# Optimization experiments

Measured on AMD Instinct MI355X. Metric: run time of the kernel, lower is better.

The kernel has to match this reference:

```python
import jax, jax.numpy as jnp
import numpy as np

ASSIGN_TEMP = 0.1
BATCH_SIZE = 16
NUM_PROTOTYPES = 1024
EMBD_DIM = 512


def setup_inputs() -> dict:
    key = jax.random.key(0)
    k1, k2 = jax.random.split(key)
    feature_maps = jax.random.normal(k1, (BATCH_SIZE, EMBD_DIM, 64, 64), dtype=jnp.float32)
    prototypes = jax.random.normal(k2, (1, NUM_PROTOTYPES, EMBD_DIM), dtype=jnp.float32)
    return {"feature_maps": feature_maps, "prototypes": prototypes}


def reference(feature_maps, prototypes):
    # assign_nearest_clusters
    bs, c, h, w = feature_maps.shape
    K = prototypes.shape[1]
    # [N, c] pixel embeddings (channels-last flatten, as movedim(1,3).reshape)
    x = feature_maps.transpose(0, 2, 3, 1).reshape(-1, c)
    p = prototypes[0]  # [K, c]
    d2 = (jnp.sum(x * x, axis=1, keepdims=True)
          + jnp.sum(p * p, axis=1)[None, :]
          - 2.0 * (x @ p.T))
    dist = jnp.sqrt(jnp.maximum(d2, 0.0))  # [N, K]
    sims = jax.nn.softmax(-dist / ASSIGN_TEMP, axis=1)  # [N, K]
    sims = sims.reshape(bs, h, w, K).transpose(0, 3, 1, 2)  # [bs, K, h, w]
    nearest = jnp.argmax(sims, axis=1)  # [bs, h, w]
    onehot = jax.nn.one_hot(nearest, K, dtype=jnp.int32)  # [bs, h, w, K]
    counts = onehot.sum(axis=(1, 2))  # [bs, K] pixels per prototype
    mask = (counts > 3).sum()
    return sims, mask.astype(jnp.float32) / BATCH_SIZE
```

## Files before the change

kernel.cpp:

```cpp
#include <hip/hip_runtime.h>
#include <hip/hip_bf16.h>
#include <stdint.h>

typedef _Float16 f16x8 __attribute__((ext_vector_type(8)));
typedef _Float16 f16x4 __attribute__((ext_vector_type(4)));
typedef _Float16 f16x2 __attribute__((ext_vector_type(2)));
typedef float    f32x4 __attribute__((ext_vector_type(4)));

#define NPROTO 1024
#define EMB    512
#define NB     16
#define HW     4096
#define NPIX   (NB * HW)
#define INV_TEMP 10.0f

__global__ void prep_protos(const float* __restrict__ proto,
                            _Float16* __restrict__ Ph,
                            float* __restrict__ pnorm) {
    int k = blockIdx.x;
    int t = threadIdx.x;
    const float* src = proto + (size_t)k * EMB + t * 8;
    float4 v0 = ((const float4*)src)[0];
    float4 v1 = ((const float4*)src)[1];
    float sq = v0.x*v0.x + v0.y*v0.y + v0.z*v0.z + v0.w*v0.w
             + v1.x*v1.x + v1.y*v1.y + v1.z*v1.z + v1.w*v1.w;
    f16x8 h;
    h[0] = (_Float16)v0.x; h[1] = (_Float16)v0.y; h[2] = (_Float16)v0.z; h[3] = (_Float16)v0.w;
    h[4] = (_Float16)v1.x; h[5] = (_Float16)v1.y; h[6] = (_Float16)v1.z; h[7] = (_Float16)v1.w;
    *(f16x8*)(Ph + (size_t)k * EMB + t * 8) = h;
#pragma unroll
    for (int m = 1; m < 64; m <<= 1) sq += __shfl_xor(sq, m);
    if (t == 0) pnorm[k] = sq;
}

__global__ void zero_counts(int* __restrict__ counts) {
    int i = blockIdx.x * blockDim.x + threadIdx.x;
    if (i < NB * NPROTO) counts[i] = 0;
}

__global__ __launch_bounds__(1024)
void p0_transpose(const float* __restrict__ fm, _Float16* __restrict__ Xh,
                  float* __restrict__ xn) {
    __shared__ __align__(16) unsigned char tile[128 * 1024];
    __shared__ float xnpart[32 * 128];

    const int t   = threadIdx.x;
    const int b   = blockIdx.x >> 5;
    const int px0 = (blockIdx.x & 31) * 128;

    float sq0 = 0.f, sq1 = 0.f, sq2 = 0.f, sq3 = 0.f;
    const int p4 = t & 31;
#pragma unroll
    for (int j = 0; j < 16; ++j) {
        int f4 = j * 1024 + t;
        int c  = f4 >> 5;
        float4 v = *(const float4*)(fm + ((size_t)b * EMB + c) * HW + px0 + p4 * 4);
        sq0 += v.x * v.x; sq1 += v.y * v.y; sq2 += v.z * v.z; sq3 += v.w * v.w;
#pragma unroll
        for (int i = 0; i < 4; ++i) {
            int p = p4 * 4 + i;
            float val = (i == 0) ? v.x : (i == 1) ? v.y : (i == 2) ? v.z : v.w;
            int slot = (c >> 3) ^ ((p >> 2) & 63);
            *(_Float16*)(tile + p * 1024 + slot * 16 + (c & 7) * 2) = (_Float16)val;
        }
    }
    xnpart[(t >> 5) * 128 + p4 * 4 + 0] = sq0;
    xnpart[(t >> 5) * 128 + p4 * 4 + 1] = sq1;
    xnpart[(t >> 5) * 128 + p4 * 4 + 2] = sq2;
    xnpart[(t >> 5) * 128 + p4 * 4 + 3] = sq3;
    __syncthreads();

    if (t < 128) {
        float s = 0.f;
#pragma unroll
        for (int g = 0; g < 32; ++g) s += xnpart[g * 128 + t];
        xn[b * HW + px0 + t] = s;
    }
    const int wid = t >> 6, lane = t & 63;
#pragma unroll
    for (int rr = 0; rr < 8; ++rr) {
        int p = wid * 8 + rr;
        int phys = lane ^ ((p >> 2) & 63);
        f16x8 v = *(const f16x8*)(tile + p * 1024 + phys * 16);
        *(f16x8*)(Xh + ((size_t)b * HW + px0 + p) * EMB + lane * 8) = v;
    }
}

__global__ __launch_bounds__(512, 4)
void pA_gemm(const _Float16* __restrict__ Xh, const _Float16* __restrict__ Ph,
             const float* __restrict__ pnorm, const float* __restrict__ xn,
             _Float16* __restrict__ e_out, float4* __restrict__ pstat) {
    __shared__ __align__(16) unsigned char smem[74752];
    float* pn = (float*)(smem + 73728);
    float* redmax = (float*)(smem);
    float* redsum = (float*)(smem + 2048);
    float* argv_  = (float*)(smem + 4096);
    int*   argk_  = (int*)(smem + 6144);

    const int t    = threadIdx.x;
    const int lane = t & 63, wid = t >> 6;
    const int kw   = wid >> 1, pw = wid & 1;
    const int lrow = lane >> 4, lcol = lane & 15;

    const int bid   = blockIdx.x;
    const int pt    = bid >> 2, slice = bid & 3;
    const int gpx0  = pt * 128;
    const int k0g   = slice * 256;

    if (t < 256) pn[t] = pnorm[k0g + t];

    f32x4 acc[4][4];
#pragma unroll
    for (int i = 0; i < 4; ++i)
#pragma unroll
        for (int j = 0; j < 4; ++j)
#pragma unroll
            for (int e = 0; e < 4; ++e) acc[i][j][e] = 0.0f;

    auto stage = [&](int buf, int ks) {
        const int c0 = ks * 32;
        unsigned char* base = smem + buf * 24576;
#pragma unroll
        for (int h = 0; h < 2; ++h) {
            int r  = wid * 32 + h * 16 + (lane >> 2);
            int cg = (lane & 3) ^ ((r >> 1) & 3);
            __builtin_amdgcn_global_load_lds(
                (const __attribute__((address_space(1))) void*)(Ph + (size_t)(k0g + r) * EMB + c0 + cg * 8),
                (__attribute__((address_space(3))) void*)(base + wid * 2048 + h * 1024),
                16, 0, 0);
        }
        int px  = wid * 16 + (lane >> 2);
        int cgb = (lane & 3) ^ ((px >> 1) & 3);
        __builtin_amdgcn_global_load_lds(
            (const __attribute__((address_space(1))) void*)(Xh + (size_t)(gpx0 + px) * EMB + c0 + cgb * 8),
            (__attribute__((address_space(3))) void*)(base + 16384 + wid * 1024),
            16, 0, 0);
    };

    stage(0, 0);
    stage(1, 1);
    asm volatile("s_waitcnt vmcnt(3)" ::: "memory");
    __builtin_amdgcn_s_barrier();
    __builtin_amdgcn_sched_barrier(0);

#pragma unroll
    for (int ks = 0; ks < 16; ++ks) {
        const int buf = ks % 3;
        if (ks < 14) stage((ks + 2) % 3, ks + 2);
        const unsigned char* Ab = smem + buf * 24576;
        const unsigned char* Bb = Ab + 16384;

        f16x8 bf[4];
#pragma unroll
        for (int nf = 0; nf < 4; ++nf) {
            int px = pw * 64 + nf * 16 + lcol;
            bf[nf] = *(const f16x8*)(Bb + px * 64 + ((lrow ^ ((px >> 1) & 3)) << 4));
        }
        __builtin_amdgcn_s_setprio(1);
#pragma unroll
        for (int mf = 0; mf < 4; ++mf) {
            int r = kw * 64 + mf * 16 + lcol;
            f16x8 af = *(const f16x8*)(Ab + r * 64 + ((lrow ^ ((r >> 1) & 3)) << 4));
#pragma unroll
            for (int nf = 0; nf < 4; ++nf)
                acc[mf][nf] = __builtin_amdgcn_mfma_f32_16x16x32_f16(af, bf[nf], acc[mf][nf], 0, 0, 0);
        }
        __builtin_amdgcn_s_setprio(0);

        if (ks < 14) {
            asm volatile("s_waitcnt vmcnt(3)" ::: "memory");
        } else if (ks == 14) {
            asm volatile("s_waitcnt vmcnt(0)" ::: "memory");
        }
        if (ks < 15) {
            __builtin_amdgcn_s_barrier();
            __builtin_amdgcn_sched_barrier(0);
        }
    }

    float xnv[4];
#pragma unroll
    for (int nf = 0; nf < 4; ++nf) xnv[nf] = xn[gpx0 + pw * 64 + nf * 16 + lcol];

    float lmax[4] = {-1e30f, -1e30f, -1e30f, -1e30f};
    float lav[4]  = {-1e30f, -1e30f, -1e30f, -1e30f};
    int   lak[4]  = {0, 0, 0, 0};
#pragma unroll
    for (int mf = 0; mf < 4; ++mf)
#pragma unroll
        for (int nf = 0; nf < 4; ++nf)
#pragma unroll
            for (int j = 0; j < 4; ++j) {
                int kl = kw * 64 + mf * 16 + lrow * 4 + j;
                float d2 = xnv[nf] + pn[kl] - 2.0f * acc[mf][nf][j];
                float lg = -INV_TEMP * sqrtf(fmaxf(d2, 0.0f));
                acc[mf][nf][j] = lg;
                if (lg > lav[nf]) { lav[nf] = lg; lak[nf] = kl; }
                lmax[nf] = fmaxf(lmax[nf], lg);
            }
#pragma unroll
    for (int nf = 0; nf < 4; ++nf)
#pragma unroll
        for (int m = 16; m <= 32; m <<= 1) {
            float ov = __shfl_xor(lav[nf], m);
            int   ok = __shfl_xor(lak[nf], m);
            if (ov > lav[nf] || (ov == lav[nf] && ok < lak[nf])) { lav[nf] = ov; lak[nf] = ok; }
            lmax[nf] = fmaxf(lmax[nf], __shfl_xor(lmax[nf], m));
        }

    __syncthreads();
    if (lane < 16)
#pragma unroll
        for (int nf = 0; nf < 4; ++nf) {
            int px = pw * 64 + nf * 16 + lane;
            redmax[kw * 128 + px] = lmax[nf];
            argv_[kw * 128 + px]  = lav[nf];
            argk_[kw * 128 + px]  = lak[nf];
        }
    __syncthreads();

#pragma unroll
    for (int nf = 0; nf < 4; ++nf) {
        int px = pw * 64 + nf * 16 + lcol;
        float m = -1e30f;
#pragma unroll
        for (int w = 0; w < 4; ++w) m = fmaxf(m, redmax[w * 128 + px]);
        float s = 0.0f;
#pragma unroll
        for (int mf = 0; mf < 4; ++mf)
#pragma unroll
            for (int j = 0; j < 4; ++j) {
                float e = __expf(acc[mf][nf][j] - m);
                acc[mf][nf][j] = e;
                s += e;
            }
        s += __shfl_xor(s, 16);
        s += __shfl_xor(s, 32);
        if (lane < 16) redsum[kw * 128 + nf * 16 + pw * 64 + lane] = s;
    }

#pragma unroll
    for (int mf = 0; mf < 4; ++mf)
#pragma unroll
        for (int nf = 0; nf < 4; ++nf) {
            int px = pw * 64 + nf * 16 + lcol;
            int kl = kw * 64 + mf * 16 + lrow * 4;
            f16x4 h;
#pragma unroll
            for (int j = 0; j < 4; ++j) h[j] = (_Float16)acc[mf][nf][j];
            *(f16x4*)(e_out + (size_t)(gpx0 + px) * NPROTO + k0g + kl) = h;
        }
    __syncthreads();

    if (kw == 0 && lane < 16) {
#pragma unroll
        for (int nf = 0; nf < 4; ++nf) {
            int px = pw * 64 + nf * 16 + lane;
            float m = -1e30f, s = 0.0f, av = -1e30f;
            int ak = 0;
#pragma unroll
            for (int w = 0; w < 4; ++w) {
                m = fmaxf(m, redmax[w * 128 + px]);
                s += redsum[w * 128 + px];
                float v = argv_[w * 128 + px];
                int   k = argk_[w * 128 + px];
                if (v > av || (v == av && k < ak)) { av = v; ak = k; }
            }
            float4 st;
            st.x = m; st.y = s; st.z = __int_as_float(k0g + ak); st.w = 0.0f;
            pstat[(size_t)slice * NPIX + gpx0 + px] = st;
        }
    }
}

__global__ void pC_combine(const float4* __restrict__ pstat, float* __restrict__ scale,
                           int* __restrict__ counts) {
    int px = blockIdx.x * 256 + threadIdx.x;
    if (px >= NPIX) return;
    float4 s0 = pstat[px];
    float4 s1 = pstat[NPIX + px];
    float4 s2 = pstat[2 * NPIX + px];
    float4 s3 = pstat[3 * NPIX + px];
    float m = fmaxf(fmaxf(s0.x, s1.x), fmaxf(s2.x, s3.x));
    float e0 = __expf(s0.x - m), e1 = __expf(s1.x - m);
    float e2 = __expf(s2.x - m), e3 = __expf(s3.x - m);
    float S = s0.y * e0 + s1.y * e1 + s2.y * e2 + s3.y * e3;
    float rs = 1.0f / S;
    scale[px * 4 + 0] = e0 * rs;
    scale[px * 4 + 1] = e1 * rs;
    scale[px * 4 + 2] = e2 * rs;
    scale[px * 4 + 3] = e3 * rs;
    float bv = s0.x; int bk = __float_as_int(s0.z);
    if (s1.x > bv) { bv = s1.x; bk = __float_as_int(s1.z); }
    if (s2.x > bv) { bv = s2.x; bk = __float_as_int(s2.z); }
    if (s3.x > bv) { bv = s3.x; bk = __float_as_int(s3.z); }
    int b = px >> 12;
    atomicAdd(&counts[b * NPROTO + bk], 1);
}

__global__ __launch_bounds__(1024)
void pB_emit(const _Float16* __restrict__ e, const float* __restrict__ scale,
             float* __restrict__ out) {
    __shared__ float tile[64 * 261];

    const int t = threadIdx.x;
    const int px0g = blockIdx.x * 256;
    const int b = px0g >> 12, hw0 = px0g & 4095;
    const int lpx = t >> 2, kq = t & 3;
    const int orow = t >> 4, oseg = t & 15;

    for (int kc = 0; kc < 16; ++kc) {
        int slice = kc >> 2;
        float sc = scale[(px0g + lpx) * 4 + slice];
        const _Float16* src = e + (size_t)(px0g + lpx) * NPROTO + kc * 64 + kq * 16;
        f16x8 h0 = *(const f16x8*)(src);
        f16x8 h1 = *(const f16x8*)(src + 8);
        if (kc) __syncthreads();
#pragma unroll
        for (int j = 0; j < 8; ++j) {
            tile[(kq * 16 + j) * 261 + lpx]     = (float)h0[j] * sc;
            tile[(kq * 16 + 8 + j) * 261 + lpx] = (float)h1[j] * sc;
        }
        __syncthreads();
        size_t obase = (size_t)b * NPROTO * HW + (size_t)(kc * 64 + orow) * HW + hw0 + oseg * 16;
#pragma unroll
        for (int i = 0; i < 4; ++i) {
            float4 v;
            v.x = tile[orow * 261 + oseg * 16 + i * 4 + 0];
            v.y = tile[orow * 261 + oseg * 16 + i * 4 + 1];
            v.z = tile[orow * 261 + oseg * 16 + i * 4 + 2];
            v.w = tile[orow * 261 + oseg * 16 + i * 4 + 3];
            *(float4*)(out + obase + i * 4) = v;
        }
    }
}

__global__ void finalize(const int* __restrict__ counts, float* __restrict__ out) {
    int t = threadIdx.x;
    int local = 0;
    for (int i = t; i < NB * NPROTO; i += 256) local += (counts[i] > 3) ? 1 : 0;
#pragma unroll
    for (int m = 1; m < 64; m <<= 1) local += __shfl_xor(local, m);
    __shared__ int wsum[4];
    if ((t & 63) == 0) wsum[t >> 6] = local;
    __syncthreads();
    if (t == 0) out[(size_t)NPIX * NPROTO] = (float)(wsum[0] + wsum[1] + wsum[2] + wsum[3]) / 16.0f;
}

__global__ __launch_bounds__(1024, 1)
void assign_fused(const float* __restrict__ fm, const _Float16* __restrict__ Ph,
                  const float* __restrict__ pnorm, int* __restrict__ counts,
                  float* __restrict__ out) {
    __shared__ __align__(16) unsigned char smem[143360];
    unsigned char* Abuf = smem;
    unsigned char* Bbuf = smem + 131072;
    float* pn           = (float*)(smem + 139264);
    float* redmax = (float*)(smem);
    float* redsum = (float*)(smem + 4096);
    float* argv_  = (float*)(smem + 8192);
    int*   argk_  = (int*)  (smem + 12288);
    float* xnsum  = (float*)(smem + 16384);
    float* xn     = (float*)(smem + 20480);

    const int t    = threadIdx.x;
    const int lane = t & 63, wid = t >> 6;
    const int lrow = lane >> 4, lcol = lane & 15;
    const int n0  = blockIdx.x * 64;
    const int b   = n0 >> 12;
    const int hw0 = n0 & 4095;

    pn[t] = pnorm[t];
    f32x4 acc[4][4];
#pragma unroll
    for (int i = 0; i < 4; ++i)
#pragma unroll
        for (int j = 0; j < 4; ++j)
#pragma unroll
            for (int e = 0; e < 4; ++e) acc[i][j][e] = 0.0f;

    const int bpx = t & 63;
    const int bc  = (t >> 6) << 1;
    const float* fmB = fm + (size_t)b * EMB * HW + hw0 + bpx;
    float sq = 0.0f;
    float bv0, bv1;

    auto stageA = [&](int cur, int ks) {
        const int c0 = ks * 32;
#pragma unroll
        for (int p = 0; p < 4; ++p) {
            int k  = p * 256 + wid * 16 + (lane >> 2);
            int cg = (lane & 3) ^ (k & 3);
            __builtin_amdgcn_global_load_lds(
                (const __attribute__((address_space(1))) void*)(Ph + (size_t)k * EMB + c0 + cg * 8),
                (__attribute__((address_space(3))) void*)(Abuf + cur * 65536 + p * 16384 + wid * 1024),
                16, 0, 0);
        }
    };
    auto loadB = [&](int ks) {
        const float* p0 = fmB + (size_t)(ks * 32 + bc) * HW;
        bv0 = p0[0]; bv1 = p0[HW];
    };
    auto writeB = [&](int cur) {
        sq += bv0 * bv0 + bv1 * bv1;
        f16x2 h; h[0] = (_Float16)bv0; h[1] = (_Float16)bv1;
        int slot = (bc >> 3) ^ (bpx & 3);
        *(f16x2*)(Bbuf + cur * 4096 + bpx * 64 + (slot << 4) + (bc & 7) * 2) = h;
    };

    stageA(0, 0); loadB(0); writeB(0);
    __syncthreads();
    int cur = 0;
    for (int ks = 0; ks < 16; ++ks) {
        if (ks < 15) { stageA(cur ^ 1, ks + 1); loadB(ks + 1); }
        f16x8 bf[4];
#pragma unroll
        for (int nf = 0; nf < 4; ++nf) {
            int px = nf * 16 + lcol;
            bf[nf] = *(const f16x8*)(Bbuf + cur * 4096 + px * 64 + ((lrow ^ (px & 3)) << 4));
        }
#pragma unroll
        for (int mf = 0; mf < 4; ++mf) {
            int r = wid * 64 + mf * 16 + lcol;
            f16x8 af = *(const f16x8*)(Abuf + cur * 65536 + r * 64 + ((lrow ^ (r & 3)) << 4));
#pragma unroll
            for (int nf = 0; nf < 4; ++nf)
                acc[mf][nf] = __builtin_amdgcn_mfma_f32_16x16x32_f16(af, bf[nf], acc[mf][nf], 0, 0, 0);
        }
        if (ks < 15) writeB(cur ^ 1);
        __syncthreads();
        cur ^= 1;
    }

    xnsum[(t >> 6) * 64 + bpx] = sq;
    __syncthreads();
    if (t < 64) {
        float s = 0.0f;
#pragma unroll
        for (int g = 0; g < 16; ++g) s += xnsum[g * 64 + t];
        xn[t] = s;
    }
    __syncthreads();

    float xnv[4];
#pragma unroll
    for (int nf = 0; nf < 4; ++nf) xnv[nf] = xn[nf * 16 + lcol];
    float lmax[4] = {-1e30f, -1e30f, -1e30f, -1e30f};
    float lav[4]  = {-1e30f, -1e30f, -1e30f, -1e30f};
    int   lak[4]  = {0, 0, 0, 0};
#pragma unroll
    for (int mf = 0; mf < 4; ++mf)
#pragma unroll
        for (int nf = 0; nf < 4; ++nf)
#pragma unroll
            for (int j = 0; j < 4; ++j) {
                int kidx = wid * 64 + mf * 16 + lrow * 4 + j;
                float d2 = xnv[nf] + pn[kidx] - 2.0f * acc[mf][nf][j];
                float lg = -INV_TEMP * sqrtf(fmaxf(d2, 0.0f));
                acc[mf][nf][j] = lg;
                if (lg > lav[nf]) { lav[nf] = lg; lak[nf] = kidx; }
                lmax[nf] = fmaxf(lmax[nf], lg);
            }
#pragma unroll
    for (int nf = 0; nf < 4; ++nf)
#pragma unroll
        for (int m = 16; m <= 32; m <<= 1) {
            float ov = __shfl_xor(lav[nf], m);
            int   ok = __shfl_xor(lak[nf], m);
            if (ov > lav[nf] || (ov == lav[nf] && ok < lak[nf])) { lav[nf] = ov; lak[nf] = ok; }
            lmax[nf] = fmaxf(lmax[nf], __shfl_xor(lmax[nf], m));
        }
    if (lane < 16)
#pragma unroll
        for (int nf = 0; nf < 4; ++nf) {
            int idx = wid * 64 + nf * 16 + lane;
            redmax[idx] = lmax[nf]; argv_[idx] = lav[nf]; argk_[idx] = lak[nf];
        }
    __syncthreads();

#pragma unroll
    for (int nf = 0; nf < 4; ++nf) {
        int px = nf * 16 + lcol;
        float gm = -1e30f, gav = -1e30f;
        int gak = 0;
#pragma unroll
        for (int w = 0; w < 16; ++w) {
            gm = fmaxf(gm, redmax[w * 64 + px]);
            float av = argv_[w * 64 + px];
            int   ak = argk_[w * 64 + px];
            if (av > gav || (av == gav && ak < gak)) { gav = av; gak = ak; }
        }
        if (wid == 0 && lane < 16) atomicAdd(&counts[b * NPROTO + gak], 1);
        float s = 0.0f;
#pragma unroll
        for (int mf = 0; mf < 4; ++mf)
#pragma unroll
            for (int j = 0; j < 4; ++j) {
                float e = __expf(acc[mf][nf][j] - gm);
                acc[mf][nf][j] = e;
                s += e;
            }
        s += __shfl_xor(s, 16);
        s += __shfl_xor(s, 32);
        if (lane < 16) redsum[wid * 64 + nf * 16 + lane] = s;
    }
    __syncthreads();

    const size_t obase = (size_t)b * NPROTO * HW + hw0;
#pragma unroll
    for (int nf = 0; nf < 4; ++nf) {
        int px = nf * 16 + lcol;
        float s = 0.0f;
#pragma unroll
        for (int w = 0; w < 16; ++w) s += redsum[w * 64 + px];
        float inv = 1.0f / s;
#pragma unroll
        for (int mf = 0; mf < 4; ++mf)
#pragma unroll
            for (int j = 0; j < 4; ++j) {
                int kidx = wid * 64 + mf * 16 + lrow * 4 + j;
                out[obase + (size_t)kidx * HW + px] = acc[mf][nf][j] * inv;
            }
    }
}

extern "C" void kernel_launch(void* const* d_in, const int* in_sizes, int n_in,
                              void* d_out, int out_size, void* d_ws, size_t ws_size,
                              hipStream_t stream) {
    const float* fm    = (const float*)d_in[0];
    const float* proto = (const float*)d_in[1];
    float* out = (float*)d_out;

    char* ws = (char*)d_ws;
    const size_t E_OFF  = 0;
    const size_t XH_OFF = 134217728;
    const size_t PS_OFF = XH_OFF + 67108864;
    const size_t SC_OFF = PS_OFF + 4194304;
    const size_t XN_OFF = SC_OFF + 1048576;
    const size_t PH_OFF = XN_OFF + 262144;
    const size_t PN_OFF = PH_OFF + 1048576;
    const size_t CT_OFF = PN_OFF + 4096;
    const size_t NEED   = CT_OFF + 65536;

    if (ws_size >= NEED) {
        _Float16* e     = (_Float16*)(ws + E_OFF);
        _Float16* Xh    = (_Float16*)(ws + XH_OFF);
        float4*   pstat = (float4*)(ws + PS_OFF);
        float*    scale = (float*)(ws + SC_OFF);
        float*    xn    = (float*)(ws + XN_OFF);
        _Float16* Ph    = (_Float16*)(ws + PH_OFF);
        float*    pnorm = (float*)(ws + PN_OFF);
        int*      counts= (int*)(ws + CT_OFF);

        prep_protos<<<NPROTO, 64, 0, stream>>>(proto, Ph, pnorm);
        zero_counts<<<(NB * NPROTO + 255) / 256, 256, 0, stream>>>(counts);
        p0_transpose<<<NB * 32, 1024, 0, stream>>>(fm, Xh, xn);
        pA_gemm<<<(NPIX / 128) * 4, 512, 0, stream>>>(Xh, Ph, pnorm, xn, e, pstat);
        pC_combine<<<NPIX / 256, 256, 0, stream>>>(pstat, scale, counts);
        pB_emit<<<NPIX / 256, 1024, 0, stream>>>(e, scale, out);
        finalize<<<1, 256, 0, stream>>>(counts, out);
    } else {
        _Float16* Ph    = (_Float16*)ws;
        float*    pnorm = (float*)(ws + (size_t)NPROTO * EMB * 2);
        int*      counts= (int*)(ws + (size_t)NPROTO * EMB * 2 + 4096);
        prep_protos<<<NPROTO, 64, 0, stream>>>(proto, Ph, pnorm);
        zero_counts<<<(NB * NPROTO + 255) / 256, 256, 0, stream>>>(counts);
        assign_fused<<<NPIX / 64, 1024, 0, stream>>>(fm, Ph, pnorm, counts, out);
        finalize<<<1, 256, 0, stream>>>(counts, out);
    }
}
```

Baseline: 329.2 us.

## Enlarge GEMM tile to 256x256 with 64-wide K steps and phased staging

Reworks the distance GEMM to compute a 256-pixel by 256-prototype tile per 512-thread block, with a 64-element K step, double-buffered LDS and XOR swizzling. Each K step is split into four phases that interleave global-to-LDS staging of the next tile with MFMA work on the current one. The intent is more operand reuse per LDS load and fewer blocks and barriers. The softmax max is now taken from the argmax value rather than a separate max reduction, and the square root uses an inline v_sqrt. In exchange the block needs about 129 KB of LDS and twice the accumulator registers, which limits occupancy to two blocks.

```diff
diff --git a/kernel.cpp b/kernel.cpp
--- a/kernel.cpp
+++ b/kernel.cpp
@@ -86,118 +86,155 @@
     }
 }
 
-__global__ __launch_bounds__(512, 4)
+__global__ __launch_bounds__(512, 2)
 void pA_gemm(const _Float16* __restrict__ Xh, const _Float16* __restrict__ Ph,
              const float* __restrict__ pnorm, const float* __restrict__ xn,
              _Float16* __restrict__ e_out, float4* __restrict__ pstat) {
-    __shared__ __align__(16) unsigned char smem[74752];
-    float* pn = (float*)(smem + 73728);
-    float* redmax = (float*)(smem);
+    __shared__ __align__(16) unsigned char smem[132096];
+    float* pn = (float*)(smem + 131072);
     float* redsum = (float*)(smem + 2048);
     float* argv_  = (float*)(smem + 4096);
     int*   argk_  = (int*)(smem + 6144);
 
     const int t    = threadIdx.x;
     const int lane = t & 63, wid = t >> 6;
-    const int kw   = wid >> 1, pw = wid & 1;
+    const int kw   = wid >> 2, pw = wid & 3;
     const int lrow = lane >> 4, lcol = lane & 15;
 
-    const int bid   = blockIdx.x;
-    const int pt    = bid >> 2, slice = bid & 3;
-    const int gpx0  = pt * 128;
+    const int pt    = blockIdx.x & 255, slice = blockIdx.x >> 8;
+    const int gpx0  = pt * 256;
     const int k0g   = slice * 256;
 
     if (t < 256) pn[t] = pnorm[k0g + t];
 
-    f32x4 acc[4][4];
-#pragma unroll
-    for (int i = 0; i < 4; ++i)
+    f32x4 acc[8][4];
+#pragma unroll
+    for (int i = 0; i < 8; ++i)
 #pragma unroll
         for (int j = 0; j < 4; ++j)
 #pragma unroll
             for (int e = 0; e < 4; ++e) acc[i][j][e] = 0.0f;
 
-    auto stage = [&](int buf, int ks) {
-        const int c0 = ks * 32;
-        unsigned char* base = smem + buf * 24576;
-#pragma unroll
-        for (int h = 0; h < 2; ++h) {
-            int r  = wid * 32 + h * 16 + (lane >> 2);
-            int cg = (lane & 3) ^ ((r >> 1) & 3);
+    const int srow8 = t >> 3, sslot = t & 7;
+    auto stage_half = [&](int buf, int kt, int half) {
+#pragma unroll
+        for (int r2 = 0; r2 < 2; ++r2) {
+            int row = (half & 1) * 128 + r2 * 64 + srow8;
+            int cg  = sslot ^ (row & 7);
+            const _Float16* src = (half >= 2)
+                ? (Xh + (size_t)(gpx0 + row) * EMB + kt * 64 + cg * 8)
+                : (Ph + (size_t)(k0g + row) * EMB + kt * 64 + cg * 8);
             __builtin_amdgcn_global_load_lds(
-                (const __attribute__((address_space(1))) void*)(Ph + (size_t)(k0g + r) * EMB + c0 + cg * 8),
-                (__attribute__((address_space(3))) void*)(base + wid * 2048 + h * 1024),
+                (const __attribute__((address_space(1))) void*)src,
+                (__attribute__((address_space(3))) void*)(smem + buf * 65536 +
+                    ((half >= 2) ? 32768 : 0) + row * 128 + sslot * 16),
                 16, 0, 0);
         }
-        int px  = wid * 16 + (lane >> 2);
-        int cgb = (lane & 3) ^ ((px >> 1) & 3);
-        __builtin_amdgcn_global_load_lds(
-            (const __attribute__((address_space(1))) void*)(Xh + (size_t)(gpx0 + px) * EMB + c0 + cgb * 8),
-            (__attribute__((address_space(3))) void*)(base + 16384 + wid * 1024),
-            16, 0, 0);
     };
 
-    stage(0, 0);
-    stage(1, 1);
-    asm volatile("s_waitcnt vmcnt(3)" ::: "memory");
-    __builtin_amdgcn_s_barrier();
-    __builtin_amdgcn_sched_barrier(0);
-
-#pragma unroll
-    for (int ks = 0; ks < 16; ++ks) {
-        const int buf = ks % 3;
-        if (ks < 14) stage((ks + 2) % 3, ks + 2);
-        const unsigned char* Ab = smem + buf * 24576;
-        const unsigned char* Bb = Ab + 16384;
-
-        f16x8 bf[4];
+    stage_half(0, 0, 0); stage_half(0, 0, 1); stage_half(0, 0, 2); stage_half(0, 0, 3);
+    __syncthreads();
+
+    const int swz0 = ((lrow)     ^ (lcol & 7)) << 4;
+    const int swz1 = ((4 + lrow) ^ (lcol & 7)) << 4;
+    const int aoff = (kw * 128 + lcol) * 128;
+    const int boff = 32768 + (pw * 64 + lcol) * 128;
+
+#pragma unroll 2
+    for (int kt = 0; kt < 8; ++kt) {
+        const unsigned char* cb = smem + (kt & 1) * 65536;
+        const int nbuf = (kt & 1) ^ 1;
+        f16x8 afr[4][2], bfr[4][2];
+
+        if (kt < 7) stage_half(nbuf, kt + 1, 0);
 #pragma unroll
         for (int nf = 0; nf < 4; ++nf) {
-            int px = pw * 64 + nf * 16 + lcol;
-            bf[nf] = *(const f16x8*)(Bb + px * 64 + ((lrow ^ ((px >> 1) & 3)) << 4));
-        }
+            bfr[nf][0] = *(const f16x8*)(cb + boff + nf * 2048 + swz0);
+            bfr[nf][1] = *(const f16x8*)(cb + boff + nf * 2048 + swz1);
+        }
+#pragma unroll
+        for (int mf = 0; mf < 4; ++mf) {
+            afr[mf][0] = *(const f16x8*)(cb + aoff + mf * 2048 + swz0);
+            afr[mf][1] = *(const f16x8*)(cb + aoff + mf * 2048 + swz1);
+        }
+        __builtin_amdgcn_s_barrier();
         __builtin_amdgcn_s_setprio(1);
 #pragma unroll
+        for (int mf = 0; mf < 4; ++mf)
+#pragma unroll
+            for (int nf = 0; nf < 2; ++nf) {
+                acc[mf][nf] = __builtin_amdgcn_mfma_f32_16x16x32_f16(afr[mf][0], bfr[nf][0], acc[mf][nf], 0, 0, 0);
+                acc[mf][nf] = __builtin_amdgcn_mfma_f32_16x16x32_f16(afr[mf][1], bfr[nf][1], acc[mf][nf], 0, 0, 0);
+            }
+        __builtin_amdgcn_s_setprio(0);
+        __builtin_amdgcn_s_barrier();
+
+        if (kt < 7) stage_half(nbuf, kt + 1, 1);
+        __builtin_amdgcn_s_setprio(1);
+#pragma unroll
+        for (int mf = 0; mf < 4; ++mf)
+#pragma unroll
+            for (int nf = 2; nf < 4; ++nf) {
+                acc[mf][nf] = __builtin_amdgcn_mfma_f32_16x16x32_f16(afr[mf][0], bfr[nf][0], acc[mf][nf], 0, 0, 0);
+                acc[mf][nf] = __builtin_amdgcn_mfma_f32_16x16x32_f16(afr[mf][1], bfr[nf][1], acc[mf][nf], 0, 0, 0);
+            }
+        __builtin_amdgcn_s_setprio(0);
+        __builtin_amdgcn_s_barrier();
+
+        if (kt < 7) stage_half(nbuf, kt + 1, 2);
+#pragma unroll
         for (int mf = 0; mf < 4; ++mf) {
-            int r = kw * 64 + mf * 16 + lcol;
-            f16x8 af = *(const f16x8*)(Ab + r * 64 + ((lrow ^ ((r >> 1) & 3)) << 4));
-#pragma unroll
-            for (int nf = 0; nf < 4; ++nf)
-                acc[mf][nf] = __builtin_amdgcn_mfma_f32_16x16x32_f16(af, bf[nf], acc[mf][nf], 0, 0, 0);
-        }
+            afr[mf][0] = *(const f16x8*)(cb + aoff + (mf + 4) * 2048 + swz0);
+            afr[mf][1] = *(const f16x8*)(cb + aoff + (mf + 4) * 2048 + swz1);
+        }
+        __builtin_amdgcn_s_barrier();
+        __builtin_amdgcn_s_setprio(1);
+#pragma unroll
+        for (int mf = 0; mf < 4; ++mf)
+#pragma unroll
+            for (int nf = 0; nf < 2; ++nf) {
+                acc[mf + 4][nf] = __builtin_amdgcn_mfma_f32_16x16x32_f16(afr[mf][0], bfr[nf][0], acc[mf + 4][nf], 0, 0, 0);
+                acc[mf + 4][nf] = __builtin_amdgcn_mfma_f32_16x16x32_f16(afr[mf][1], bfr[nf][1], acc[mf + 4][nf], 0, 0, 0);
+            }
         __builtin_amdgcn_s_setprio(0);
-
-        if (ks < 14) {
-            asm volatile("s_waitcnt vmcnt(3)" ::: "memory");
-        } else if (ks == 14) {
-            asm volatile("s_waitcnt vmcnt(0)" ::: "memory");
-        }
-        if (ks < 15) {
-            __builtin_amdgcn_s_barrier();
-            __builtin_amdgcn_sched_barrier(0);
-        }
+        __builtin_amdgcn_s_barrier();
+
+        if (kt < 7) stage_half(nbuf, kt + 1, 3);
+        __builtin_amdgcn_s_setprio(1);
+#pragma unroll
+        for (int mf = 0; mf < 4; ++mf)
+#pragma unroll
+            for (int nf = 2; nf < 4; ++nf) {
+                acc[mf + 4][nf] = __builtin_amdgcn_mfma_f32_16x16x32_f16(afr[mf][0], bfr[nf][0], acc[mf + 4][nf], 0, 0, 0);
+                acc[mf + 4][nf] = __builtin_amdgcn_mfma_f32_16x16x32_f16(afr[mf][1], bfr[nf][1], acc[mf + 4][nf], 0, 0, 0);
+            }
+        __builtin_amdgcn_s_setprio(0);
+        __syncthreads();
     }
 
     float xnv[4];
 #pragma unroll
     for (int nf = 0; nf < 4; ++nf) xnv[nf] = xn[gpx0 + pw * 64 + nf * 16 + lcol];
 
-    float lmax[4] = {-1e30f, -1e30f, -1e30f, -1e30f};
-    float lav[4]  = {-1e30f, -1e30f, -1e30f, -1e30f};
-    int   lak[4]  = {0, 0, 0, 0};
-#pragma unroll
-    for (int mf = 0; mf < 4; ++mf)
+    float lav[4] = {-1e30f, -1e30f, -1e30f, -1e30f};
+    int   lak[4] = {0, 0, 0, 0};
+#pragma unroll
+    for (int mf = 0; mf < 8; ++mf) {
+        const int klb = kw * 128 + mf * 16 + lrow * 4;
+        float4 pn4 = *(const float4*)(pn + klb);
 #pragma unroll
         for (int nf = 0; nf < 4; ++nf)
 #pragma unroll
             for (int j = 0; j < 4; ++j) {
-                int kl = kw * 64 + mf * 16 + lrow * 4 + j;
-                float d2 = xnv[nf] + pn[kl] - 2.0f * acc[mf][nf][j];
-                float lg = -INV_TEMP * sqrtf(fmaxf(d2, 0.0f));
+                float pnj = (j == 0) ? pn4.x : (j == 1) ? pn4.y : (j == 2) ? pn4.z : pn4.w;
+                float d2 = fmaxf(xnv[nf] + pnj - 2.0f * acc[mf][nf][j], 0.0f);
+                float sq;
+                asm("v_sqrt_f32 %0, %1" : "=v"(sq) : "v"(d2));
+                float lg = -INV_TEMP * sq;
                 acc[mf][nf][j] = lg;
-                if (lg > lav[nf]) { lav[nf] = lg; lak[nf] = kl; }
-                lmax[nf] = fmaxf(lmax[nf], lg);
-            }
+                if (lg > lav[nf]) { lav[nf] = lg; lak[nf] = klb + j; }
+            }
+    }
 #pragma unroll
     for (int nf = 0; nf < 4; ++nf)
 #pragma unroll
@@ -205,29 +242,23 @@
             float ov = __shfl_xor(lav[nf], m);
             int   ok = __shfl_xor(lak[nf], m);
             if (ov > lav[nf] || (ov == lav[nf] && ok < lak[nf])) { lav[nf] = ov; lak[nf] = ok; }
-            lmax[nf] = fmaxf(lmax[nf], __shfl_xor(lmax[nf], m));
-        }
-
-    __syncthreads();
+        }
     if (lane < 16)
 #pragma unroll
         for (int nf = 0; nf < 4; ++nf) {
             int px = pw * 64 + nf * 16 + lane;
-            redmax[kw * 128 + px] = lmax[nf];
-            argv_[kw * 128 + px]  = lav[nf];
-            argk_[kw * 128 + px]  = lak[nf];
+            argv_[kw * 256 + px] = lav[nf];
+            argk_[kw * 256 + px] = lak[nf];
         }
     __syncthreads();
 
 #pragma unroll
     for (int nf = 0; nf < 4; ++nf) {
         int px = pw * 64 + nf * 16 + lcol;
-        float m = -1e30f;
-#pragma unroll
-        for (int w = 0; w < 4; ++w) m = fmaxf(m, redmax[w * 128 + px]);
+        float m = fmaxf(argv_[px], argv_[256 + px]);
         float s = 0.0f;
 #pragma unroll
-        for (int mf = 0; mf < 4; ++mf)
+        for (int mf = 0; mf < 8; ++mf)
 #pragma unroll
             for (int j = 0; j < 4; ++j) {
                 float e = __expf(acc[mf][nf][j] - m);
@@ -236,15 +267,15 @@
             }
         s += __shfl_xor(s, 16);
         s += __shfl_xor(s, 32);
-        if (lane < 16) redsum[kw * 128 + nf * 16 + pw * 64 + lane] = s;
-    }
-
-#pragma unroll
-    for (int mf = 0; mf < 4; ++mf)
+        if (lane < 16) redsum[kw * 256 + nf * 16 + pw * 64 + lane] = s;
+    }
+
+#pragma unroll
+    for (int mf = 0; mf < 8; ++mf)
 #pragma unroll
         for (int nf = 0; nf < 4; ++nf) {
             int px = pw * 64 + nf * 16 + lcol;
-            int kl = kw * 64 + mf * 16 + lrow * 4;
+            int kl = kw * 128 + mf * 16 + lrow * 4;
             f16x4 h;
 #pragma unroll
             for (int j = 0; j < 4; ++j) h[j] = (_Float16)acc[mf][nf][j];
@@ -256,18 +287,12 @@
 #pragma unroll
         for (int nf = 0; nf < 4; ++nf) {
             int px = pw * 64 + nf * 16 + lane;
-            float m = -1e30f, s = 0.0f, av = -1e30f;
-            int ak = 0;
-#pragma unroll
-            for (int w = 0; w < 4; ++w) {
-                m = fmaxf(m, redmax[w * 128 + px]);
-                s += redsum[w * 128 + px];
-                float v = argv_[w * 128 + px];
-                int   k = argk_[w * 128 + px];
-                if (v > av || (v == av && k < ak)) { av = v; ak = k; }
-            }
+            float av = argv_[px]; int ak = argk_[px];
+            float a1 = argv_[256 + px]; int k1 = argk_[256 + px];
+            if (a1 > av) { av = a1; ak = k1; }
+            float s = redsum[px] + redsum[256 + px];
             float4 st;
-            st.x = m; st.y = s; st.z = __int_as_float(k0g + ak); st.w = 0.0f;
+            st.x = av; st.y = s; st.z = __int_as_float(k0g + ak); st.w = 0.0f;
             pstat[(size_t)slice * NPIX + gpx0 + px] = st;
         }
     }
@@ -554,7 +579,7 @@
         prep_protos<<<NPROTO, 64, 0, stream>>>(proto, Ph, pnorm);
         zero_counts<<<(NB * NPROTO + 255) / 256, 256, 0, stream>>>(counts);
         p0_transpose<<<NB * 32, 1024, 0, stream>>>(fm, Xh, xn);
-        pA_gemm<<<(NPIX / 128) * 4, 512, 0, stream>>>(Xh, Ph, pnorm, xn, e, pstat);
+        pA_gemm<<<(NPIX / 256) * 4, 512, 0, stream>>>(Xh, Ph, pnorm, xn, e, pstat);
         pC_combine<<<NPIX / 256, 256, 0, stream>>>(pstat, scale, counts);
         pB_emit<<<NPIX / 256, 1024, 0, stream>>>(e, scale, out);
         finalize<<<1, 256, 0, stream>>>(counts, out);
```

New measurement: 370.3 us. 1.12x slower.
